# Kernel optimization log

Measured on AMD Instinct MI355X. Metric: run time of the kernel, lower is better.

The kernel has to match this reference:

```python
import jax, jax.numpy as jnp
import numpy as np
import itertools

NUM_BITS = 32
ORDER = 2
BATCH = 131072


def _build_padded_indices():
    """All combinations of bit positions up to ORDER, padded with sentinel NUM_BITS.

    The sentinel points at an extra spin column fixed to +1, so the padded
    product equals the ragged reduce_prod of the original TF code.
    """
    combos = []
    for i in range(1, ORDER + 1):
        combos.extend(itertools.combinations(range(NUM_BITS), i))
    num_vars = len(combos)  # 528 for (32, 2)
    idx = np.full((num_vars, ORDER), NUM_BITS, dtype=np.int32)
    for r, c in enumerate(combos):
        idx[r, : len(c)] = c
    return idx


def setup_inputs() -> dict:
    key = jax.random.key(0)
    k1, k2 = jax.random.split(key)
    bitstrings = jax.random.randint(k1, (BATCH, NUM_BITS), 0, 2, dtype=jnp.int32)
    # keras RandomUniform default: U(-0.05, 0.05)
    variables = jax.random.uniform(k2, (528,), dtype=jnp.float32,
                                   minval=-0.05, maxval=0.05)
    indices = jnp.asarray(_build_padded_indices())
    return {"bitstrings": bitstrings, "variables": variables, "indices": indices}


def reference(bitstrings, variables, indices):
    # spins in {+1, -1}
    spins = (1 - 2 * bitstrings).astype(jnp.float32)               # [B, n]
    ones = jnp.ones((spins.shape[0], 1), dtype=spins.dtype)
    spins_ext = jnp.concatenate([spins, ones], axis=-1)            # [B, n+1]
    gathered = spins_ext[:, indices]                               # [B, V, ORDER]
    parities = jnp.prod(gathered, axis=-1)                         # [B, V]
    return jnp.einsum('bv,v->b', parities, variables)              # [B]
```

## Files before the change

### kernel.cpp

```cpp
#include <hip/hip_runtime.h>


constexpr int NB = 32;

__global__ __launch_bounds__(256) void KOBE_76948634075865_kernel(
    const int* __restrict__ bits,
    const float* __restrict__ vars,
    float* __restrict__ out,
    int n) {
  int b = blockIdx.x * 256 + threadIdx.x;
  if (b >= n) return;

  const int4* row = reinterpret_cast<const int4*>(bits) + (size_t)b * (NB / 4);
  float s[NB];
#pragma unroll
  for (int k = 0; k < NB / 4; ++k) {
    int4 q = row[k];
    s[4 * k + 0] = __int_as_float(0x3f800000u ^ ((unsigned)q.x << 31));
    s[4 * k + 1] = __int_as_float(0x3f800000u ^ ((unsigned)q.y << 31));
    s[4 * k + 2] = __int_as_float(0x3f800000u ^ ((unsigned)q.z << 31));
    s[4 * k + 3] = __int_as_float(0x3f800000u ^ ((unsigned)q.w << 31));
  }

  float acc = 0.f;
  int p = NB;
#pragma unroll
  for (int i = 0; i < NB; ++i) {
    float gi = vars[i];
#pragma unroll
    for (int j = i + 1; j < NB; ++j) {
      gi = fmaf(vars[p], s[j], gi);
      ++p;
    }
    acc = fmaf(s[i], gi, acc);
  }
  out[b] = acc;
}

extern "C" void kernel_launch(void* const* d_in, const int* in_sizes, int n_in,
                              void* d_out, int out_size, void* d_ws, size_t ws_size,
                              hipStream_t stream) {
  const int* bits = (const int*)d_in[0];
  const float* vars = (const float*)d_in[1];
  float* out = (float*)d_out;
  int n = in_sizes[0] / NB;
  int blocks = (n + 255) / 256;
  KOBE_76948634075865_kernel<<<blocks, 256, 0, stream>>>(bits, vars, out, n);
}
```

Before: 70.67 us.

## Load bitstrings coalesced and pack rows into bitmasks via wave ballot

Replaces each thread's strided per-row int4 loads with fully coalesced block-wide loads: each of 32 passes reads 256 consecutive ints, and a wave ballot packs every 32-int row into a 32-bit mask stored in shared memory. Each thread then reads its row's mask and expands the bits into +/-1 spins. This targets poor coalescing of the 128-byte-strided per-thread loads, at the cost of 32 ballots, LDS writes and a block barrier.

New measurement: 78.49 us. 1.11x slower.

```diff
diff --git a/kernel.cpp b/kernel.cpp
--- a/kernel.cpp
+++ b/kernel.cpp
@@ -8,18 +8,39 @@
     const float* __restrict__ vars,
     float* __restrict__ out,
     int n) {
-  int b = blockIdx.x * 256 + threadIdx.x;
-  if (b >= n) return;
+  __shared__ unsigned smask[256];
 
-  const int4* row = reinterpret_cast<const int4*>(bits) + (size_t)b * (NB / 4);
+  const int t = threadIdx.x;
+  const int lane = t & 63;
+  const int w = t >> 6;
+
+  const long long tile_row0 = (long long)blockIdx.x * 256;
+  const long long tile_int0 = tile_row0 * NB;
+  const long long total_ints = (long long)n * NB;
+  const int* __restrict__ tile = bits + tile_int0;
+
+#pragma unroll
+  for (int k = 0; k < 32; ++k) {
+    const int off = k * 256 + t;
+    int v = 0;
+    if (tile_int0 + off < total_ints) v = tile[off];
+    const unsigned long long bal = __ballot(v != 0);
+    if ((lane & 31) == 0) {
+      const int r0 = k * 8 + w * 2 + (lane >> 5);
+      smask[r0] = (unsigned)(bal >> (lane & 32));
+    }
+  }
+  __syncthreads();
+
+  const long long row = tile_row0 + t;
+  if (row >= n) return;
+
+  const unsigned x = smask[t];
+
   float s[NB];
 #pragma unroll
-  for (int k = 0; k < NB / 4; ++k) {
-    int4 q = row[k];
-    s[4 * k + 0] = __int_as_float(0x3f800000u ^ ((unsigned)q.x << 31));
-    s[4 * k + 1] = __int_as_float(0x3f800000u ^ ((unsigned)q.y << 31));
-    s[4 * k + 2] = __int_as_float(0x3f800000u ^ ((unsigned)q.z << 31));
-    s[4 * k + 3] = __int_as_float(0x3f800000u ^ ((unsigned)q.w << 31));
+  for (int i = 0; i < NB; ++i) {
+    s[i] = __int_as_float(0x3f800000u ^ ((x << (31 - i)) & 0x80000000u));
   }
 
   float acc = 0.f;
@@ -34,7 +55,7 @@
     }
     acc = fmaf(s[i], gi, acc);
   }
-  out[b] = acc;
+  out[row] = acc;
 }
 
 extern "C" void kernel_launch(void* const* d_in, const int* in_sizes, int n_in,
```
